# Optimization experiments

Measured on AMD Instinct MI355X. Metric: run time of the kernel, lower is better.

## Reference

```python
import jax, jax.numpy as jnp
import numpy as np

B, C, H, W = 4, 64, 64, 64

def _conv1x1(x, w, b):
    # Conv2d(k=1): y[b,o,h,w] = sum_c x[b,c,h,w]*w[o,c] + b[o]
    return jnp.einsum('bchw,oc->bohw', x, w) + b[None, :, None, None]

def setup_inputs() -> dict:
    key = jax.random.key(0)
    ks = jax.random.split(key, 8)
    s = 1.0 / np.sqrt(C)
    return {
        'v1': jax.random.normal(ks[0], (B, C, H, W), jnp.float32),
        'v2': jax.random.normal(ks[1], (B, C, H, W), jnp.float32),
        'wq': jax.random.normal(ks[2], (C, C), jnp.float32) * s,
        'bq': jax.random.normal(ks[3], (C,), jnp.float32) * 0.01,
        'wk': jax.random.normal(ks[4], (C, C), jnp.float32) * s,
        'bk': jax.random.normal(ks[5], (C,), jnp.float32) * 0.01,
        'wv': jax.random.normal(ks[6], (C, C), jnp.float32) * s,
        'bv': jax.random.normal(ks[7], (C,), jnp.float32) * 0.01,
    }

def reference(v1, v2, wq, bq, wk, bk, wv, bv):
    q = _conv1x1(v1, wq, bq)   # (B,C,H,W)
    k = _conv1x1(v2, wk, bk)
    v = _conv1x1(v2, wv, bv)
    b, c, h, w = q.shape
    n = c * h                   # tokens = C*H, feature dim = W (matches torch view)
    qf = q.reshape(b, n, w)
    kf = k.reshape(b, n, w)
    vf = v.reshape(b, n, w)
    scores = jnp.einsum('bnw,bmw->bnm', qf, kf)   # (B, N, N)
    attn = jax.nn.softmax(scores, axis=-1)
    out = jnp.einsum('bnm,bmw->bnw', attn, vf)
    return out.reshape(v1.shape)
```

## Files before the change

### kernel.cpp

```cpp
#include <hip/hip_runtime.h>


#define Bn 4
#define Cc 64
#define HW 4096
#define Nn 4096
#define Dd 64
#define TS (Bn * Nn * Dd)
#define LOG2E 1.44269504088896340736f

typedef _Float16 f16;
typedef _Float16 f16x8 __attribute__((ext_vector_type(8)));
typedef _Float16 f16x4 __attribute__((ext_vector_type(4)));
typedef __fp16 fp16x2 __attribute__((ext_vector_type(2)));
typedef float f32x4 __attribute__((ext_vector_type(4)));

__device__ __forceinline__ int swz(int row, int col) {
    return row * 64 + (col ^ ((row & 7) << 3));
}

__device__ __forceinline__ void gl_lds16(const f16* g, f16* l) {
    __builtin_amdgcn_global_load_lds(
        (const __attribute__((address_space(1))) unsigned int*)g,
        (__attribute__((address_space(3))) unsigned int*)l, 16, 0, 0);
}

__global__ __launch_bounds__(256) void qkv_conv(
    const float* __restrict__ v1, const float* __restrict__ v2,
    const float* __restrict__ wq, const float* __restrict__ bq,
    const float* __restrict__ wk, const float* __restrict__ bk,
    const float* __restrict__ wv, const float* __restrict__ bv,
    f16* __restrict__ Qh, f16* __restrict__ Kh, f16* __restrict__ Vh)
{
    const int t    = threadIdx.x;
    const int lane = t & 63;
    const int og   = __builtin_amdgcn_readfirstlane(t >> 6);
    const int b    = blockIdx.y;
    const int p    = blockIdx.x * 64 + lane;
    const int z    = blockIdx.z;
    const int zt   = z >> 1;
    const int ch0  = (z & 1) * 32 + og * 8;

    const float* w    = (zt == 0) ? wq : (zt == 1) ? wk : wv;
    const float* bias = (zt == 0) ? bq : (zt == 1) ? bk : bv;
    const float* x    = ((zt == 0) ? v1 : v2) + (size_t)b * (Cc * HW) + p;

    float acc[8];
    #pragma unroll
    for (int j = 0; j < 8; ++j) acc[j] = bias[ch0 + j];
    #pragma unroll 16
    for (int c = 0; c < 64; ++c) {
        float xc = x[c * HW];
        #pragma unroll
        for (int j = 0; j < 8; ++j)
            acc[j] = fmaf(w[(ch0 + j) * 64 + c], xc, acc[j]);
    }

    f16* dst = (zt == 0) ? Qh : (zt == 1) ? Kh : Vh;
    const float scale = (zt == 0) ? LOG2E : 1.0f;
    #pragma unroll
    for (int j = 0; j < 8; ++j) {
        size_t idx = (size_t)b * (Nn * Dd) + (size_t)(ch0 + j) * 4096 + p;
        dst[idx] = (f16)(acc[j] * scale);
    }
}

__global__ __launch_bounds__(256) void vtrans(const f16* __restrict__ Vh,
                                              f16* __restrict__ Vt)
{
    __shared__ f16 tile[64][72];
    const int t  = threadIdx.x;
    const int n0 = blockIdx.x * 64;
    const int b  = blockIdx.y;
    for (int i = t; i < 4096; i += 256) {
        int r = i >> 6, c = i & 63;
        tile[r][c] = Vh[(size_t)b * (Nn * Dd) + (size_t)(n0 + r) * 64 + c];
    }
    __syncthreads();
    for (int i = t; i < 4096; i += 256) {
        int w = i >> 6, n = i & 63;
        Vt[(size_t)b * (Dd * Nn) + (size_t)w * Nn + n0 + n] = tile[n][w];
    }
}

__global__ __launch_bounds__(512, 4) void attn(
    const f16* __restrict__ Qhg, const f16* __restrict__ Khg,
    const f16* __restrict__ Vtg,
    float* __restrict__ out, f16* __restrict__ Opart, float2* __restrict__ ml)
{
    __shared__ __align__(16) f16 KT[2][4096];
    __shared__ __align__(16) f16 VT[2][4096];

    const int t    = threadIdx.x;
    const int lane = t & 63, wvi = t >> 6;
    const int g = lane >> 4, c = lane & 15;
    const int b  = blockIdx.z;
    const int sp = blockIdx.y;
    const int S  = gridDim.y;
    const int n0 = blockIdx.x * 256;
    const int keysPerSplit = Nn / S;
    const int nTiles = keysPerSplit / 64;
    const int kbase = sp * keysPerSplit;

    const int srow = t >> 3;
    const int gc   = ((t & 7) ^ (srow & 7)) * 8;
    f16* ldsKdst0 = &KT[0][(wvi * 8) * 64];
    f16* ldsKdst1 = &KT[1][(wvi * 8) * 64];
    f16* ldsVdst0 = &VT[0][(wvi * 8) * 64];
    f16* ldsVdst1 = &VT[1][(wvi * 8) * 64];

    const f16* Kb = Khg + (size_t)b * (Nn * Dd);
    const f16* Vb = Vtg + (size_t)b * (Dd * Nn);

    f16x8 qbh[2][2];
    #pragma unroll
    for (int qf = 0; qf < 2; ++qf) {
        const int qrow = n0 + wvi * 32 + qf * 16 + c;
        const f16* qhp = Qhg + ((size_t)b * Nn + qrow) * 64;
        #pragma unroll
        for (int ks = 0; ks < 2; ++ks)
            qbh[qf][ks] = *(const f16x8*)(qhp + ks * 32 + g * 8);
    }

    float m_run[2] = {-1e30f, -1e30f}, lpart[2] = {0.f, 0.f};
    f32x4 of[2][4];
    #pragma unroll
    for (int qf = 0; qf < 2; ++qf)
        #pragma unroll
        for (int nf = 0; nf < 4; ++nf)
            #pragma unroll
            for (int r = 0; r < 4; ++r) of[qf][nf][r] = 0.f;

    gl_lds16(Kb + (size_t)(kbase + srow) * 64 + gc, ldsKdst0);
    gl_lds16(Vb + (size_t)srow * Nn + kbase + gc, ldsVdst0);
    __syncthreads();
    int cur = 0;

    for (int kt = 0; kt < nTiles; ++kt) {
        if (kt + 1 < nTiles) {
            const int k0n = kbase + (kt + 1) * 64;
            f16* kd = cur ? ldsKdst0 : ldsKdst1;
            f16* vd = cur ? ldsVdst0 : ldsVdst1;
            gl_lds16(Kb + (size_t)(k0n + srow) * 64 + gc, kd);
            gl_lds16(Vb + (size_t)srow * Nn + k0n + gc, vd);
        }

        const f16* KTc = KT[cur];
        const f16* VTc = VT[cur];

        f32x4 accS[2][4];
        #pragma unroll
        for (int qf = 0; qf < 2; ++qf)
            #pragma unroll
            for (int fm = 0; fm < 4; ++fm)
                #pragma unroll
                for (int r = 0; r < 4; ++r) accS[qf][fm][r] = 0.f;
        #pragma unroll
        for (int fm = 0; fm < 4; ++fm) {
            const int key = fm * 16 + c;
            f16x8 kh0 = *(const f16x8*)(KTc + swz(key, g * 8));
            f16x8 kh1 = *(const f16x8*)(KTc + swz(key, 32 + g * 8));
            #pragma unroll
            for (int qf = 0; qf < 2; ++qf) {
                accS[qf][fm] = __builtin_amdgcn_mfma_f32_16x16x32_f16(kh0, qbh[qf][0], accS[qf][fm], 0, 0, 0);
                accS[qf][fm] = __builtin_amdgcn_mfma_f32_16x16x32_f16(kh1, qbh[qf][1], accS[qf][fm], 0, 0, 0);
            }
        }

        f16x4 pb[2][4];
        #pragma unroll
        for (int qf = 0; qf < 2; ++qf) {
            float m0 = fmaxf(fmaxf(accS[qf][0][0], accS[qf][0][1]),
                             fmaxf(accS[qf][0][2], accS[qf][0][3]));
            float m1 = fmaxf(fmaxf(accS[qf][1][0], accS[qf][1][1]),
                             fmaxf(accS[qf][1][2], accS[qf][1][3]));
            float m2 = fmaxf(fmaxf(accS[qf][2][0], accS[qf][2][1]),
                             fmaxf(accS[qf][2][2], accS[qf][2][3]));
            float m3 = fmaxf(fmaxf(accS[qf][3][0], accS[qf][3][1]),
                             fmaxf(accS[qf][3][2], accS[qf][3][3]));
            float tmax = fmaxf(fmaxf(m0, m1), fmaxf(m2, m3));
            tmax = fmaxf(tmax, __shfl_xor(tmax, 16));
            tmax = fmaxf(tmax, __shfl_xor(tmax, 32));
            if (!__all(tmax <= m_run[qf] + 8.f)) {
                const float mnew = fmaxf(m_run[qf], tmax);
                const float corr = exp2f(m_run[qf] - mnew);
                lpart[qf] *= corr;
                #pragma unroll
                for (int nf = 0; nf < 4; ++nf)
                    #pragma unroll
                    for (int r = 0; r < 4; ++r) of[qf][nf][r] *= corr;
                m_run[qf] = mnew;
            }
            float s01 = 0.f, s23 = 0.f;
            #pragma unroll
            for (int fm = 0; fm < 4; ++fm) {
                #pragma unroll
                for (int r = 0; r < 4; ++r) {
                    float pp = exp2f(accS[qf][fm][r] - m_run[qf]);
                    accS[qf][fm][r] = pp;
                    if (fm < 2) s01 += pp; else s23 += pp;
                }
                union { f16x4 v4; fp16x2 h2[2]; } u;
                u.h2[0] = __builtin_amdgcn_cvt_pkrtz(accS[qf][fm][0], accS[qf][fm][1]);
                u.h2[1] = __builtin_amdgcn_cvt_pkrtz(accS[qf][fm][2], accS[qf][fm][3]);
                pb[qf][fm] = u.v4;
            }
            lpart[qf] += s01 + s23;
        }

        #pragma unroll
        for (int nf = 0; nf < 4; ++nf) {
            #pragma unroll
            for (int fm = 0; fm < 4; ++fm) {
                f16x4 va = *(const f16x4*)(VTc + swz(nf * 16 + c, fm * 16 + g * 4));
                of[0][nf] = __builtin_amdgcn_mfma_f32_16x16x16f16(va, pb[0][fm], of[0][nf], 0, 0, 0);
                of[1][nf] = __builtin_amdgcn_mfma_f32_16x16x16f16(va, pb[1][fm], of[1][nf], 0, 0, 0);
            }
        }

        __syncthreads();
        cur ^= 1;
    }

    if (S == 1) {
        #pragma unroll
        for (int qf = 0; qf < 2; ++qf) {
            float lr = lpart[qf];
            lr += __shfl_xor(lr, 16);
            lr += __shfl_xor(lr, 32);
            const float linv = 1.0f / lr;
            const int n = n0 + wvi * 32 + qf * 16 + c;
            #pragma unroll
            for (int nf = 0; nf < 4; ++nf) {
                float4 o4 = make_float4(of[qf][nf][0] * linv, of[qf][nf][1] * linv,
                                        of[qf][nf][2] * linv, of[qf][nf][3] * linv);
                *(float4*)(out + (((size_t)b * Nn + n) << 6) + nf * 16 + g * 4) = o4;
            }
        }
    } else {
        #pragma unroll
        for (int qf = 0; qf < 2; ++qf) {
            float lr = lpart[qf];
            lr += __shfl_xor(lr, 16);
            lr += __shfl_xor(lr, 32);
            const float linv = 1.0f / lr;
            const int n = n0 + wvi * 32 + qf * 16 + c;
            size_t robase = (((size_t)sp * Bn + b) * Nn + n) << 6;
            #pragma unroll
            for (int nf = 0; nf < 4; ++nf) {
                union { f16x4 v4; fp16x2 h2[2]; } u;
                u.h2[0] = __builtin_amdgcn_cvt_pkrtz(of[qf][nf][0] * linv, of[qf][nf][1] * linv);
                u.h2[1] = __builtin_amdgcn_cvt_pkrtz(of[qf][nf][2] * linv, of[qf][nf][3] * linv);
                *(f16x4*)(Opart + robase + nf * 16 + g * 4) = u.v4;
            }
            if (g == 0) {
                ml[((size_t)sp * Bn + b) * Nn + n] = make_float2(m_run[qf], lr);
            }
        }
    }
}

__global__ __launch_bounds__(256) void combine(
    const f16* __restrict__ Opart, const float2* __restrict__ ml,
    float* __restrict__ out, int S)
{
    const int idx8 = blockIdx.x * 256 + threadIdx.x;
    const int w8 = idx8 & 7;
    const int n  = (idx8 >> 3) & (Nn - 1);
    const int b  = idx8 >> 15;
    float M = -1e30f;
    for (int s = 0; s < S; ++s)
        M = fmaxf(M, ml[((size_t)s * Bn + b) * Nn + n].x);
    float num[8];
    #pragma unroll
    for (int j = 0; j < 8; ++j) num[j] = 0.f;
    float den = 0.f;
    for (int s = 0; s < S; ++s) {
        float2 m2 = ml[((size_t)s * Bn + b) * Nn + n];
        float a = exp2f(m2.x - M) * m2.y;
        f16x8 o8 = *(const f16x8*)(Opart + ((((size_t)s * Bn + b) * Nn + n) << 6) + w8 * 8);
        #pragma unroll
        for (int j = 0; j < 8; ++j) num[j] += a * (float)o8[j];
        den += a;
    }
    const float di = 1.0f / den;
    float* op = out + (((size_t)b * Nn + n) << 6) + w8 * 8;
    float4 lo = make_float4(num[0] * di, num[1] * di, num[2] * di, num[3] * di);
    float4 hi = make_float4(num[4] * di, num[5] * di, num[6] * di, num[7] * di);
    *(float4*)op = lo;
    *(float4*)(op + 4) = hi;
}

extern "C" void kernel_launch(void* const* d_in, const int* in_sizes, int n_in,
                              void* d_out, int out_size, void* d_ws, size_t ws_size,
                              hipStream_t stream)
{
    const float* v1 = (const float*)d_in[0];
    const float* v2 = (const float*)d_in[1];
    const float* wq = (const float*)d_in[2];
    const float* bq = (const float*)d_in[3];
    const float* wk = (const float*)d_in[4];
    const float* bk = (const float*)d_in[5];
    const float* wv = (const float*)d_in[6];
    const float* bv = (const float*)d_in[7];
    float* out = (float*)d_out;

    char* ws = (char*)d_ws;
    const size_t T = (size_t)TS * sizeof(f16);
    f16* Qh = (f16*)(ws + 0 * T);
    f16* Kh = (f16*)(ws + 1 * T);
    f16* Vh = (f16*)(ws + 2 * T);
    f16* Vt = (f16*)(ws + 3 * T);
    const size_t base = 4 * T;
    const size_t opartBytes = (size_t)TS * 2;
    const size_t mlBytes    = (size_t)Bn * Nn * 8;

    int S = 1;
    if      (ws_size >= base + 8 * (opartBytes + mlBytes)) S = 8;
    else if (ws_size >= base + 4 * (opartBytes + mlBytes)) S = 4;
    else if (ws_size >= base + 2 * (opartBytes + mlBytes)) S = 2;

    f16*    Opart = (f16*)(ws + base);
    float2* mlp   = (float2*)(ws + base + (size_t)S * opartBytes);

    qkv_conv<<<dim3(64, 4, 6), 256, 0, stream>>>(v1, v2, wq, bq, wk, bk, wv, bv,
                                                 Qh, Kh, Vh);
    vtrans<<<dim3(64, 4), 256, 0, stream>>>(Vh, Vt);
    attn<<<dim3(16, S, 4), 512, 0, stream>>>(Qh, Kh, Vt, out, Opart, mlp);
    if (S > 1) {
        combine<<<(Bn * Nn * Dd / 8) / 256, 256, 0, stream>>>(Opart, mlp, out, S);
    }
}
```

Before: 71.19 us.

## Process key tiles in pairs per barrier and compute row sums via MFMA

The key loop now loads and processes two 64-key tiles per iteration, with double-buffered pairs in LDS. This halves the number of __syncthreads barriers and lengthens the overlap window for the async loads. The softmax row sum moves from scalar adds plus cross-lane shuffles to an MFMA against a vector of ones, which offloads VALU work to the matrix unit. In exchange, LDS use doubles to 64KB per block, which may reduce occupancy. The fp16-rounded probabilities are now what gets summed, and the code assumes an even number of tiles per split.

New measurement: 77.77 us. 9.2% more time.

```diff
diff --git a/kernel.cpp b/kernel.cpp
--- a/kernel.cpp
+++ b/kernel.cpp
@@ -88,8 +88,8 @@
     const f16* __restrict__ Vtg,
     float* __restrict__ out, f16* __restrict__ Opart, float2* __restrict__ ml)
 {
-    __shared__ __align__(16) f16 KT[2][4096];
-    __shared__ __align__(16) f16 VT[2][4096];
+    __shared__ __align__(16) f16 KT[2][2][4096];
+    __shared__ __align__(16) f16 VT[2][2][4096];
 
     const int t    = threadIdx.x;
     const int lane = t & 63, wvi = t >> 6;
@@ -100,14 +100,12 @@
     const int n0 = blockIdx.x * 256;
     const int keysPerSplit = Nn / S;
     const int nTiles = keysPerSplit / 64;
+    const int nPairs = nTiles >> 1;
     const int kbase = sp * keysPerSplit;
 
     const int srow = t >> 3;
     const int gc   = ((t & 7) ^ (srow & 7)) * 8;
-    f16* ldsKdst0 = &KT[0][(wvi * 8) * 64];
-    f16* ldsKdst1 = &KT[1][(wvi * 8) * 64];
-    f16* ldsVdst0 = &VT[0][(wvi * 8) * 64];
-    f16* ldsVdst1 = &VT[1][(wvi * 8) * 64];
+    const int ldsoff = (wvi * 8) * 64;
 
     const f16* Kb = Khg + (size_t)b * (Nn * Dd);
     const f16* Vb = Vtg + (size_t)b * (Dd * Nn);
@@ -122,99 +120,112 @@
             qbh[qf][ks] = *(const f16x8*)(qhp + ks * 32 + g * 8);
     }
 
-    float m_run[2] = {-1e30f, -1e30f}, lpart[2] = {0.f, 0.f};
+    const f16x4 ones = {(f16)1.f, (f16)1.f, (f16)1.f, (f16)1.f};
+
+    float m_run[2] = {-1e30f, -1e30f};
+    f32x4 lacc[2];
     f32x4 of[2][4];
     #pragma unroll
-    for (int qf = 0; qf < 2; ++qf)
+    for (int qf = 0; qf < 2; ++qf) {
+        #pragma unroll
+        for (int r = 0; r < 4; ++r) lacc[qf][r] = 0.f;
         #pragma unroll
         for (int nf = 0; nf < 4; ++nf)
             #pragma unroll
             for (int r = 0; r < 4; ++r) of[qf][nf][r] = 0.f;
-
-    gl_lds16(Kb + (size_t)(kbase + srow) * 64 + gc, ldsKdst0);
-    gl_lds16(Vb + (size_t)srow * Nn + kbase + gc, ldsVdst0);
+    }
+
+    #pragma unroll
+    for (int sub = 0; sub < 2; ++sub) {
+        const int k0 = kbase + sub * 64;
+        gl_lds16(Kb + (size_t)(k0 + srow) * 64 + gc, &KT[0][sub][ldsoff]);
+        gl_lds16(Vb + (size_t)srow * Nn + k0 + gc, &VT[0][sub][ldsoff]);
+    }
     __syncthreads();
     int cur = 0;
 
-    for (int kt = 0; kt < nTiles; ++kt) {
-        if (kt + 1 < nTiles) {
-            const int k0n = kbase + (kt + 1) * 64;
-            f16* kd = cur ? ldsKdst0 : ldsKdst1;
-            f16* vd = cur ? ldsVdst0 : ldsVdst1;
-            gl_lds16(Kb + (size_t)(k0n + srow) * 64 + gc, kd);
-            gl_lds16(Vb + (size_t)srow * Nn + k0n + gc, vd);
+    for (int p = 0; p < nPairs; ++p) {
+        if (p + 1 < nPairs) {
+            const int kp = kbase + (p + 1) * 128;
+            #pragma unroll
+            for (int sub = 0; sub < 2; ++sub) {
+                const int k0 = kp + sub * 64;
+                gl_lds16(Kb + (size_t)(k0 + srow) * 64 + gc, &KT[cur ^ 1][sub][ldsoff]);
+                gl_lds16(Vb + (size_t)srow * Nn + k0 + gc, &VT[cur ^ 1][sub][ldsoff]);
+            }
         }
 
-        const f16* KTc = KT[cur];
-        const f16* VTc = VT[cur];
-
-        f32x4 accS[2][4];
-        #pragma unroll
-        for (int qf = 0; qf < 2; ++qf)
-            #pragma unroll
-            for (int fm = 0; fm < 4; ++fm)
-                #pragma unroll
-                for (int r = 0; r < 4; ++r) accS[qf][fm][r] = 0.f;
-        #pragma unroll
-        for (int fm = 0; fm < 4; ++fm) {
-            const int key = fm * 16 + c;
-            f16x8 kh0 = *(const f16x8*)(KTc + swz(key, g * 8));
-            f16x8 kh1 = *(const f16x8*)(KTc + swz(key, 32 + g * 8));
+        #pragma unroll
+        for (int sub = 0; sub < 2; ++sub) {
+            const f16* KTc = KT[cur][sub];
+            const f16* VTc = VT[cur][sub];
+
+            f32x4 accS[2][4];
+            #pragma unroll
+            for (int qf = 0; qf < 2; ++qf)
+                #pragma unroll
+                for (int fm = 0; fm < 4; ++fm)
+                    #pragma unroll
+                    for (int r = 0; r < 4; ++r) accS[qf][fm][r] = 0.f;
+            #pragma unroll
+            for (int fm = 0; fm < 4; ++fm) {
+                const int key = fm * 16 + c;
+                f16x8 kh0 = *(const f16x8*)(KTc + swz(key, g * 8));
+                f16x8 kh1 = *(const f16x8*)(KTc + swz(key, 32 + g * 8));
+                #pragma unroll
+                for (int qf = 0; qf < 2; ++qf) {
+                    accS[qf][fm] = __builtin_amdgcn_mfma_f32_16x16x32_f16(kh0, qbh[qf][0], accS[qf][fm], 0, 0, 0);
+                    accS[qf][fm] = __builtin_amdgcn_mfma_f32_16x16x32_f16(kh1, qbh[qf][1], accS[qf][fm], 0, 0, 0);
+                }
+            }
+
+            f16x4 pb[2][4];
             #pragma unroll
             for (int qf = 0; qf < 2; ++qf) {
-                accS[qf][fm] = __builtin_amdgcn_mfma_f32_16x16x32_f16(kh0, qbh[qf][0], accS[qf][fm], 0, 0, 0);
-                accS[qf][fm] = __builtin_amdgcn_mfma_f32_16x16x32_f16(kh1, qbh[qf][1], accS[qf][fm], 0, 0, 0);
-            }
-        }
-
-        f16x4 pb[2][4];
-        #pragma unroll
-        for (int qf = 0; qf < 2; ++qf) {
-            float m0 = fmaxf(fmaxf(accS[qf][0][0], accS[qf][0][1]),
-                             fmaxf(accS[qf][0][2], accS[qf][0][3]));
-            float m1 = fmaxf(fmaxf(accS[qf][1][0], accS[qf][1][1]),
-                             fmaxf(accS[qf][1][2], accS[qf][1][3]));
-            float m2 = fmaxf(fmaxf(accS[qf][2][0], accS[qf][2][1]),
-                             fmaxf(accS[qf][2][2], accS[qf][2][3]));
-            float m3 = fmaxf(fmaxf(accS[qf][3][0], accS[qf][3][1]),
-                             fmaxf(accS[qf][3][2], accS[qf][3][3]));
-            float tmax = fmaxf(fmaxf(m0, m1), fmaxf(m2, m3));
-            tmax = fmaxf(tmax, __shfl_xor(tmax, 16));
-            tmax = fmaxf(tmax, __shfl_xor(tmax, 32));
-            if (!__all(tmax <= m_run[qf] + 8.f)) {
-                const float mnew = fmaxf(m_run[qf], tmax);
-                const float corr = exp2f(m_run[qf] - mnew);
-                lpart[qf] *= corr;
-                #pragma unroll
-                for (int nf = 0; nf < 4; ++nf)
+                float ma = fmaxf(fmaxf(accS[qf][0][0], accS[qf][0][1]), accS[qf][0][2]);
+                float mb = fmaxf(fmaxf(accS[qf][0][3], accS[qf][1][0]), accS[qf][1][1]);
+                float mc = fmaxf(fmaxf(accS[qf][1][2], accS[qf][1][3]), accS[qf][2][0]);
+                float md = fmaxf(fmaxf(accS[qf][2][1], accS[qf][2][2]), accS[qf][2][3]);
+                float me = fmaxf(fmaxf(accS[qf][3][0], accS[qf][3][1]), accS[qf][3][2]);
+                float tmax = fmaxf(fmaxf(fmaxf(ma, mb), fmaxf(mc, md)),
+                                   fmaxf(me, accS[qf][3][3]));
+                tmax = fmaxf(tmax, __shfl_xor(tmax, 16));
+                tmax = fmaxf(tmax, __shfl_xor(tmax, 32));
+                if (!__all(tmax <= m_run[qf] + 8.f)) {
+                    const float mnew = fmaxf(m_run[qf], tmax);
+                    const float corr = exp2f(m_run[qf] - mnew);
                     #pragma unroll
-                    for (int r = 0; r < 4; ++r) of[qf][nf][r] *= corr;
-                m_run[qf] = mnew;
-            }
-            float s01 = 0.f, s23 = 0.f;
-            #pragma unroll
-            for (int fm = 0; fm < 4; ++fm) {
-                #pragma unroll
-                for (int r = 0; r < 4; ++r) {
-                    float pp = exp2f(accS[qf][fm][r] - m_run[qf]);
-                    accS[qf][fm][r] = pp;
-                    if (fm < 2) s01 += pp; else s23 += pp;
+                    for (int r = 0; r < 4; ++r) lacc[qf][r] *= corr;
+                    #pragma unroll
+                    for (int nf = 0; nf < 4; ++nf)
+                        #pragma unroll
+                        for (int r = 0; r < 4; ++r) of[qf][nf][r] *= corr;
+                    m_run[qf] = mnew;
                 }
-                union { f16x4 v4; fp16x2 h2[2]; } u;
-                u.h2[0] = __builtin_amdgcn_cvt_pkrtz(accS[qf][fm][0], accS[qf][fm][1]);
-                u.h2[1] = __builtin_amdgcn_cvt_pkrtz(accS[qf][fm][2], accS[qf][fm][3]);
-                pb[qf][fm] = u.v4;
-            }
-            lpart[qf] += s01 + s23;
-        }
-
-        #pragma unroll
-        for (int nf = 0; nf < 4; ++nf) {
-            #pragma unroll
-            for (int fm = 0; fm < 4; ++fm) {
-                f16x4 va = *(const f16x4*)(VTc + swz(nf * 16 + c, fm * 16 + g * 4));
-                of[0][nf] = __builtin_amdgcn_mfma_f32_16x16x16f16(va, pb[0][fm], of[0][nf], 0, 0, 0);
-                of[1][nf] = __builtin_amdgcn_mfma_f32_16x16x16f16(va, pb[1][fm], of[1][nf], 0, 0, 0);
+                #pragma unroll
+                for (int fm = 0; fm < 4; ++fm) {
+                    float p0 = exp2f(accS[qf][fm][0] - m_run[qf]);
+                    float p1 = exp2f(accS[qf][fm][1] - m_run[qf]);
+                    float p2 = exp2f(accS[qf][fm][2] - m_run[qf]);
+                    float p3 = exp2f(accS[qf][fm][3] - m_run[qf]);
+                    union { f16x4 v4; fp16x2 h2[2]; } u;
+                    u.h2[0] = __builtin_amdgcn_cvt_pkrtz(p0, p1);
+                    u.h2[1] = __builtin_amdgcn_cvt_pkrtz(p2, p3);
+                    pb[qf][fm] = u.v4;
+                }
+                #pragma unroll
+                for (int fm = 0; fm < 4; ++fm)
+                    lacc[qf] = __builtin_amdgcn_mfma_f32_16x16x16f16(ones, pb[qf][fm], lacc[qf], 0, 0, 0);
+            }
+
+            #pragma unroll
+            for (int nf = 0; nf < 4; ++nf) {
+                #pragma unroll
+                for (int fm = 0; fm < 4; ++fm) {
+                    f16x4 va = *(const f16x4*)(VTc + swz(nf * 16 + c, fm * 16 + g * 4));
+                    of[0][nf] = __builtin_amdgcn_mfma_f32_16x16x16f16(va, pb[0][fm], of[0][nf], 0, 0, 0);
+                    of[1][nf] = __builtin_amdgcn_mfma_f32_16x16x16f16(va, pb[1][fm], of[1][nf], 0, 0, 0);
+                }
             }
         }
 
@@ -225,10 +236,7 @@
     if (S == 1) {
         #pragma unroll
         for (int qf = 0; qf < 2; ++qf) {
-            float lr = lpart[qf];
-            lr += __shfl_xor(lr, 16);
-            lr += __shfl_xor(lr, 32);
-            const float linv = 1.0f / lr;
+            const float linv = 1.0f / lacc[qf][0];
             const int n = n0 + wvi * 32 + qf * 16 + c;
             #pragma unroll
             for (int nf = 0; nf < 4; ++nf) {
@@ -240,9 +248,7 @@
     } else {
         #pragma unroll
         for (int qf = 0; qf < 2; ++qf) {
-            float lr = lpart[qf];
-            lr += __shfl_xor(lr, 16);
-            lr += __shfl_xor(lr, 32);
+            const float lr = lacc[qf][0];
             const float linv = 1.0f / lr;
             const int n = n0 + wvi * 32 + qf * 16 + c;
             size_t robase = (((size_t)sp * Bn + b) * Nn + n) << 6;
```
